# Performance work log

Measured on AMD Instinct MI355X. Metric: run time of the kernel, lower is better.

## Reference

```python
import jax, jax.numpy as jnp
import numpy as np

B, C, N, G, L = 4, 3, 1024, 2048, 32
# bound = dx/2 - bx for xbound=[-30,30,0.15], ybound=[-15,15,0.15] -> [30, 15]
BOUND = np.array([30.0, 15.0], np.float32)
THR = float(np.linalg.norm(1.5 / (2.0 * BOUND)))  # cdist_threshold in normalized coords


def _cdist(a, b):
    # torch.cdist p=2; eps keeps sqrt grad-safe (dist values only feed argmin/threshold)
    d2 = jnp.sum((a[:, None, :] - b[None, :, :]) ** 2, -1)
    return jnp.sqrt(jnp.maximum(d2, 1e-12))


def _per_class(logm, pos, gt_raw, gt_ins, gt_order):
    # logm: [N+1,N+1] log-probs, pos: [N,2] valid predicted vertices (mask all-ones),
    # gt_raw: [G,2] metric GT points, gt_ins/gt_order: [G] instance id / order in instance
    n = pos.shape[0]
    bound = jnp.asarray(BOUND, pos.dtype)
    gt = (gt_raw + bound) / (2.0 * bound)                 # normalize to [0,1]
    cd = _cdist(pos, gt)                                  # [N,G]
    nearest = jnp.argmin(cd, -1)                          # [N]
    ndist = jnp.take_along_axis(cd, nearest[:, None], 1)[:, 0]
    n_ins = jnp.where(ndist < THR, gt_ins[nearest], -1)   # matched instance or -1
    n_ord = gt_order[nearest]                             # order of matched GT point
    big = jnp.int32(1 << 20)
    ins_key = jnp.where(n_ins >= 0, n_ins, big)
    # original: per instance, sort matched pred indices by (order, index) and chain them
    order = jnp.lexsort((jnp.arange(n), n_ord, ins_key))  # sort by (ins, order, idx)
    ins_s = ins_key[order]
    same = (ins_s[:-1] == ins_s[1:]) & (ins_s[:-1] < big)
    rows = jnp.where(same, order[:-1], n)                 # dump non-links into (n,n)
    cols = jnp.where(same, order[1:], n)
    m = jnp.zeros((n + 1, n + 1), pos.dtype).at[rows, cols].set(1.0)
    mNN = m.at[n, n].set(0.0)[:n, :n]
    # conflict resolution: a column with >1 incoming keeps only the row that is
    # spatially closest to that column's vertex (torch .min -> first-index tiebreak)
    dist_pp = _cdist(pos, pos)                            # [N,N]
    colsum = mNN.sum(0)
    score = jnp.where(mNN > 0, dist_pp, jnp.inf)
    best = jnp.argmin(score, 0)                           # [N]
    mNN = ((jnp.arange(n)[:, None] == best[None, :]) & (colsum > 0)).astype(pos.dtype)
    # unmatched rows point to bin column; unmatched columns come from bin row
    to_bin = (mNN.sum(1) == 0).astype(pos.dtype)[:, None]
    from_bin = (mNN.sum(0) == 0).astype(pos.dtype)[None, :]
    match_gt = jnp.concatenate(
        [jnp.concatenate([mNN, to_bin], 1),
         jnp.concatenate([from_bin, jnp.zeros((1, 1), pos.dtype)], 1)], 0)
    idx = jnp.arange(n)
    fwd_t = jnp.argmax(match_gt, 1)[:n]                   # per-row target
    bwd_t = jnp.argmax(match_gt, 0)[:n]                   # per-col target
    # NLLLoss on transposed [1,C,d] input => -logm[j, target_j] in both cases
    mloss = -(jnp.mean(logm[idx, fwd_t]) + jnp.mean(logm[idx, bwd_t]))
    closs = jnp.mean(jnp.abs(pos - gt[nearest]))          # F.l1_loss
    return closs, mloss, match_gt


def _forward(matches, positions, gt_pts, gt_ins, gt_order):
    pos = positions[..., :-1].reshape(B * C, N, 2)
    lm = matches.reshape(B * C, N + 1, N + 1)
    gp = gt_pts.reshape(B * C, G, 2)
    gi = gt_ins.reshape(B * C, G)
    go = gt_order.reshape(B * C, G)
    closs, mloss, mgt = jax.vmap(_per_class)(lm, pos, gp, gi, go)
    # reduction='mean': mean over classes then batch == mean over all B*C
    return jnp.mean(closs), jnp.mean(mloss), mgt.reshape(B, C, N + 1, N + 1)


def setup_inputs() -> dict:
    key = jax.random.key(0)
    k1, k2, k3 = jax.random.split(key, 3)
    matches = jax.nn.log_softmax(
        jax.random.normal(k1, (B, C, N + 1, N + 1), jnp.float32), axis=-1)
    positions = jax.random.uniform(k2, (B, C, N, 3), dtype=jnp.float32)
    masks = jnp.ones((B, C, N, 1), jnp.int32)
    bound = jnp.asarray(BOUND)
    gt_pts = (jax.random.uniform(k3, (B, C, G, 2), dtype=jnp.float32) * 2.0 - 1.0) * bound
    gt_ins = jnp.broadcast_to(jnp.arange(G, dtype=jnp.int32) // L, (B, C, G))
    gt_order = jnp.broadcast_to(jnp.arange(G, dtype=jnp.int32) % L, (B, C, G))
    return {"matches": matches, "positions": positions, "masks": masks,
            "gt_pts": gt_pts, "gt_ins": gt_ins, "gt_order": gt_order}


def reference(matches, positions, masks, gt_pts, gt_ins, gt_order):
    # masks are all-ones (valid selection is identity, keeping shapes static)
    closs, mloss, matches_gt = _forward(matches, positions, gt_pts, gt_ins, gt_order)
    return closs, mloss, matches_gt
```

## Files before the change

### kernel.cpp

```cpp
#include <hip/hip_runtime.h>

#define BC 12
#define NP 1024
#define NG 2048
#define NP1 1025
#define MAT_STRIDE ((size_t)NP1 * NP1)
#define THR_F 0.05590169943749474f
#define NBLK 768
#define KEY_BIG (1 << 26)

#define WS_CLOSS 0
#define WS_MLOSS 6144
#define WS_KEY   12288

__global__ __launch_bounds__(256) void nearest_kernel(
    const float* __restrict__ positions,
    const float* __restrict__ gt_pts,
    const int* __restrict__ gt_ins,
    const int* __restrict__ gt_order,
    int* __restrict__ w_key,
    double* __restrict__ closs_part)
{
    __shared__ float4 s_gt[NG / 2];
    __shared__ double s_red[4];

    const int bx = blockIdx.x;
    const int c = bx >> 6;
    const int base = (bx & 63) * 16;
    const int tid = threadIdx.x;

    const float4* gsrc = (const float4*)(gt_pts + (size_t)c * NG * 2);
    for (int p = tid; p < NG / 2; p += 256) {
        float4 g = gsrc[p];
        g.x = (g.x + 30.0f) / 60.0f;
        g.y = (g.y + 15.0f) / 30.0f;
        g.z = (g.z + 30.0f) / 60.0f;
        g.w = (g.w + 15.0f) / 30.0f;
        s_gt[p] = g;
    }
    __syncthreads();

    const int i = base + (tid >> 4);
    const int part = tid & 15;

    const float px = positions[((size_t)c * NP + i) * 3 + 0];
    const float py = positions[((size_t)c * NP + i) * 3 + 1];

    float bd = 3.4e38f;
    int bi = 0;
    const int q0 = part * 64;
#pragma unroll 8
    for (int q = q0; q < q0 + 64; ++q) {
        float4 g = s_gt[q];
        float dx0 = px - g.x, dy0 = py - g.y;
        float d20 = __fadd_rn(__fmul_rn(dx0, dx0), __fmul_rn(dy0, dy0));
        if (d20 < bd) { bd = d20; bi = 2 * q; }
        float dx1 = px - g.z, dy1 = py - g.w;
        float d21 = __fadd_rn(__fmul_rn(dx1, dx1), __fmul_rn(dy1, dy1));
        if (d21 < bd) { bd = d21; bi = 2 * q + 1; }
    }
    for (int m = 1; m <= 8; m <<= 1) {
        float od = __shfl_xor(bd, m);
        int   oi = __shfl_xor(bi, m);
        if (od < bd || (od == bd && oi < bi)) { bd = od; bi = oi; }
    }

    double contrib = 0.0;
    if (part == 0) {
        float nd = __fsqrt_rn(fmaxf(bd, 1e-12f));
        int key;
        if (nd < THR_F) {
            int insv = gt_ins[(size_t)c * NG + bi];
            int ordv = gt_order[(size_t)c * NG + bi];
            key = (insv << 15) | (ordv << 10) | i;
        } else {
            key = KEY_BIG | i;
        }
        w_key[(size_t)c * NP + i] = key;
        float4 g = s_gt[bi >> 1];
        float gx = (bi & 1) ? g.z : g.x;
        float gy = (bi & 1) ? g.w : g.y;
        contrib = (double)fabsf(px - gx) + (double)fabsf(py - gy);
    }

    for (int off = 32; off; off >>= 1) contrib += __shfl_down(contrib, off);
    if ((tid & 63) == 0) s_red[tid >> 6] = contrib;
    __syncthreads();
    if (tid == 0)
        closs_part[bx] = s_red[0] + s_red[1] + s_red[2] + s_red[3];
}

__global__ __launch_bounds__(256) void links_kernel(
    const float* __restrict__ matches,
    const int* __restrict__ w_key,
    float* __restrict__ out,
    double* __restrict__ mloss_part)
{
    __shared__ int s_key[NP];
    __shared__ double s_red[4];

    const int bx = blockIdx.x;
    const int c = bx >> 6;
    const int base = (bx & 63) * 16;
    const int tid = threadIdx.x;

    ((int4*)s_key)[tid] = ((const int4*)(w_key + (size_t)c * NP))[tid];
    __syncthreads();

    const int i = base + (tid >> 4);
    const int part = tid & 15;
    const int ki = s_key[i];

    int succ = 0x7FFFFFFF;
    int prd = -1;
    const int4* sk4 = (const int4*)s_key;
    const int j0 = part * 16;
#pragma unroll 4
    for (int j = j0; j < j0 + 16; ++j) {
        int4 k4 = sk4[j];
        if (k4.x > ki && k4.x < succ) succ = k4.x;
        if (k4.x < ki && k4.x > prd)  prd  = k4.x;
        if (k4.y > ki && k4.y < succ) succ = k4.y;
        if (k4.y < ki && k4.y > prd)  prd  = k4.y;
        if (k4.z > ki && k4.z < succ) succ = k4.z;
        if (k4.z < ki && k4.z > prd)  prd  = k4.z;
        if (k4.w > ki && k4.w < succ) succ = k4.w;
        if (k4.w < ki && k4.w > prd)  prd  = k4.w;
    }
    for (int m = 1; m <= 8; m <<= 1) {
        int os = __shfl_xor(succ, m);
        int op = __shfl_xor(prd, m);
        if (os < succ) succ = os;
        if (op > prd)  prd  = op;
    }

    double s = 0.0;
    if (part == 0) {
        bool fl = (succ != 0x7FFFFFFF) && ((succ >> 15) == (ki >> 15)) && (ki < KEY_BIG);
        int fwd = fl ? (succ & 1023) : NP;
        bool bl = (prd >= 0) && ((prd >> 15) == (ki >> 15)) && (prd < KEY_BIG);
        int bwd = bl ? (prd & 1023) : NP;

        float* mgt = out + 2 + (size_t)c * MAT_STRIDE;
        mgt[(size_t)i * NP1 + fwd] = 1.0f;
        if (bwd == NP)
            mgt[(size_t)NP * NP1 + i] = 1.0f;
        const float* lm = matches + (size_t)c * MAT_STRIDE;
        s = (double)lm[(size_t)i * NP1 + fwd] + (double)lm[(size_t)i * NP1 + bwd];
    }

    for (int off = 32; off; off >>= 1) s += __shfl_down(s, off);
    if ((tid & 63) == 0) s_red[tid >> 6] = s;
    __syncthreads();
    if (tid == 0)
        mloss_part[bx] = s_red[0] + s_red[1] + s_red[2] + s_red[3];
}

__global__ __launch_bounds__(256) void finalize_kernel(
    const double* __restrict__ closs_part,
    const double* __restrict__ mloss_part,
    float* __restrict__ out)
{
    __shared__ double sc[4], sm[4];
    const int t = threadIdx.x;
    double cs = 0.0, ms = 0.0;
    for (int i = t; i < NBLK; i += 256) { cs += closs_part[i]; ms += mloss_part[i]; }
    for (int off = 32; off; off >>= 1) {
        cs += __shfl_down(cs, off);
        ms += __shfl_down(ms, off);
    }
    if ((t & 63) == 0) { sc[t >> 6] = cs; sm[t >> 6] = ms; }
    __syncthreads();
    if (t == 0) {
        double C = sc[0] + sc[1] + sc[2] + sc[3];
        double M = sm[0] + sm[1] + sm[2] + sm[3];
        out[0] = (float)(C / (12.0 * 2048.0));
        out[1] = (float)(-M / (12.0 * 1024.0));
    }
}

extern "C" void kernel_launch(void* const* d_in, const int* in_sizes, int n_in,
                              void* d_out, int out_size, void* d_ws, size_t ws_size,
                              hipStream_t stream) {
    const float* matches   = (const float*)d_in[0];
    const float* positions = (const float*)d_in[1];
    const float* gt_pts    = (const float*)d_in[3];
    const int*   gt_ins    = (const int*)d_in[4];
    const int*   gt_order  = (const int*)d_in[5];
    float* out = (float*)d_out;

    char* ws = (char*)d_ws;
    double* closs_part = (double*)(ws + WS_CLOSS);
    double* mloss_part = (double*)(ws + WS_MLOSS);
    int*    w_key      = (int*)(ws + WS_KEY);

    hipMemsetAsync(d_out, 0, (size_t)out_size * sizeof(float), stream);

    nearest_kernel<<<dim3(NBLK), dim3(256), 0, stream>>>(
        positions, gt_pts, gt_ins, gt_order, w_key, closs_part);
    links_kernel<<<dim3(NBLK), dim3(256), 0, stream>>>(
        matches, w_key, out, mloss_part);
    finalize_kernel<<<dim3(1), dim3(256), 0, stream>>>(
        closs_part, mloss_part, out);
}
```

Baseline: 140.3 us.

## Replace memset and scatter with a dense write kernel, interleave shared-memory loops

Drops the full-output hipMemsetAsync and the scattered 1.0 stores. The links kernel now records forward and backward indices in workspace, and a new per-row kernel writes every element of the 12×1025×1025 output once, folding the loss finalization into one block. This saves one pass over the roughly 50 MB output and removes the random-address scatter. The nearest and links loops also switch to strided indexing (t*16+part), so lanes in a group read consecutive LDS entries instead of bank-conflicting chunks. The output rows are 1025 floats, so stores are misaligned, and the finalization block adds a serial tail.

Measured after the change: 119.7 us. -14.6%, faster.

```diff
diff --git a/kernel.cpp b/kernel.cpp
--- a/kernel.cpp
+++ b/kernel.cpp
@@ -12,6 +12,8 @@
 #define WS_CLOSS 0
 #define WS_MLOSS 6144
 #define WS_KEY   12288
+#define WS_FWD   61440
+#define WS_BWD   110592
 
 __global__ __launch_bounds__(256) void nearest_kernel(
     const float* __restrict__ positions,
@@ -48,9 +50,9 @@
 
     float bd = 3.4e38f;
     int bi = 0;
-    const int q0 = part * 64;
 #pragma unroll 8
-    for (int q = q0; q < q0 + 64; ++q) {
+    for (int t = 0; t < 64; ++t) {
+        const int q = t * 16 + part;
         float4 g = s_gt[q];
         float dx0 = px - g.x, dy0 = py - g.y;
         float d20 = __fadd_rn(__fmul_rn(dx0, dx0), __fmul_rn(dy0, dy0));
@@ -93,7 +95,8 @@
 __global__ __launch_bounds__(256) void links_kernel(
     const float* __restrict__ matches,
     const int* __restrict__ w_key,
-    float* __restrict__ out,
+    int* __restrict__ w_fwd,
+    int* __restrict__ w_bwd,
     double* __restrict__ mloss_part)
 {
     __shared__ int s_key[NP];
@@ -114,9 +117,9 @@
     int succ = 0x7FFFFFFF;
     int prd = -1;
     const int4* sk4 = (const int4*)s_key;
-    const int j0 = part * 16;
 #pragma unroll 4
-    for (int j = j0; j < j0 + 16; ++j) {
+    for (int t = 0; t < 16; ++t) {
+        const int j = t * 16 + part;
         int4 k4 = sk4[j];
         if (k4.x > ki && k4.x < succ) succ = k4.x;
         if (k4.x < ki && k4.x > prd)  prd  = k4.x;
@@ -141,10 +144,8 @@
         bool bl = (prd >= 0) && ((prd >> 15) == (ki >> 15)) && (prd < KEY_BIG);
         int bwd = bl ? (prd & 1023) : NP;
 
-        float* mgt = out + 2 + (size_t)c * MAT_STRIDE;
-        mgt[(size_t)i * NP1 + fwd] = 1.0f;
-        if (bwd == NP)
-            mgt[(size_t)NP * NP1 + i] = 1.0f;
+        w_fwd[(size_t)c * NP + i] = fwd;
+        w_bwd[(size_t)c * NP + i] = bwd;
         const float* lm = matches + (size_t)c * MAT_STRIDE;
         s = (double)lm[(size_t)i * NP1 + fwd] + (double)lm[(size_t)i * NP1 + bwd];
     }
@@ -156,26 +157,51 @@
         mloss_part[bx] = s_red[0] + s_red[1] + s_red[2] + s_red[3];
 }
 
-__global__ __launch_bounds__(256) void finalize_kernel(
+__global__ __launch_bounds__(256) void write_kernel(
+    const int* __restrict__ w_fwd,
+    const int* __restrict__ w_bwd,
     const double* __restrict__ closs_part,
     const double* __restrict__ mloss_part,
     float* __restrict__ out)
 {
-    __shared__ double sc[4], sm[4];
+    const int r = blockIdx.x;
+    const int c = blockIdx.y;
     const int t = threadIdx.x;
-    double cs = 0.0, ms = 0.0;
-    for (int i = t; i < NBLK; i += 256) { cs += closs_part[i]; ms += mloss_part[i]; }
-    for (int off = 32; off; off >>= 1) {
-        cs += __shfl_down(cs, off);
-        ms += __shfl_down(ms, off);
-    }
-    if ((t & 63) == 0) { sc[t >> 6] = cs; sm[t >> 6] = ms; }
-    __syncthreads();
-    if (t == 0) {
-        double C = sc[0] + sc[1] + sc[2] + sc[3];
-        double M = sm[0] + sm[1] + sm[2] + sm[3];
-        out[0] = (float)(C / (12.0 * 2048.0));
-        out[1] = (float)(-M / (12.0 * 1024.0));
+    float* row = out + 2 + (size_t)c * MAT_STRIDE + (size_t)r * NP1;
+
+    if (r < NP) {
+        const int fwd = w_fwd[c * NP + r];
+#pragma unroll
+        for (int k = 0; k < 4; ++k) {
+            int col = t + 256 * k;
+            row[col] = (col == fwd) ? 1.0f : 0.0f;
+        }
+        if (t == 0) row[1024] = (fwd == NP) ? 1.0f : 0.0f;
+    } else {
+#pragma unroll
+        for (int k = 0; k < 4; ++k) {
+            int col = t + 256 * k;
+            row[col] = (w_bwd[c * NP + col] == NP) ? 1.0f : 0.0f;
+        }
+        if (t == 0) row[1024] = 0.0f;
+    }
+
+    if (r == 1024 && c == 0) {
+        __shared__ double sc[4], sm[4];
+        double cs = 0.0, ms = 0.0;
+        for (int i = t; i < NBLK; i += 256) { cs += closs_part[i]; ms += mloss_part[i]; }
+        for (int off = 32; off; off >>= 1) {
+            cs += __shfl_down(cs, off);
+            ms += __shfl_down(ms, off);
+        }
+        if ((t & 63) == 0) { sc[t >> 6] = cs; sm[t >> 6] = ms; }
+        __syncthreads();
+        if (t == 0) {
+            double C = sc[0] + sc[1] + sc[2] + sc[3];
+            double M = sm[0] + sm[1] + sm[2] + sm[3];
+            out[0] = (float)(C / (12.0 * 2048.0));
+            out[1] = (float)(-M / (12.0 * 1024.0));
+        }
     }
 }
 
@@ -193,13 +219,13 @@
     double* closs_part = (double*)(ws + WS_CLOSS);
     double* mloss_part = (double*)(ws + WS_MLOSS);
     int*    w_key      = (int*)(ws + WS_KEY);
-
-    hipMemsetAsync(d_out, 0, (size_t)out_size * sizeof(float), stream);
+    int*    w_fwd      = (int*)(ws + WS_FWD);
+    int*    w_bwd      = (int*)(ws + WS_BWD);
 
     nearest_kernel<<<dim3(NBLK), dim3(256), 0, stream>>>(
         positions, gt_pts, gt_ins, gt_order, w_key, closs_part);
     links_kernel<<<dim3(NBLK), dim3(256), 0, stream>>>(
-        matches, w_key, out, mloss_part);
-    finalize_kernel<<<dim3(1), dim3(256), 0, stream>>>(
-        closs_part, mloss_part, out);
-}
+        matches, w_key, w_fwd, w_bwd, mloss_part);
+    write_kernel<<<dim3(NP1, BC), dim3(256), 0, stream>>>(
+        w_fwd, w_bwd, closs_part, mloss_part, out);
+}
```
